# Optimization experiments

Measured on AMD Instinct MI355X. Metric: run time of the kernel, lower is better.

Reference implementation:

```python
import jax, jax.numpy as jnp
import numpy as np

# (top, left, bottom, right) box layout, per module constants
B, T, R, C = 32, 200, 4096, 81
REDUCTION = 16.0
IOU_THRESH = 0.7


def _make_boxes(key, b, n):
    k1, k2 = jax.random.split(key)
    cyx = jax.random.uniform(k1, (b, n, 2), minval=100.0, maxval=700.0)
    hw = jax.random.uniform(k2, (b, n, 2), minval=48.0, maxval=256.0)
    top = cyx[..., 0] - hw[..., 0] * 0.5
    left = cyx[..., 1] - hw[..., 1] * 0.5
    bottom = cyx[..., 0] + hw[..., 0] * 0.5
    right = cyx[..., 1] + hw[..., 1] * 0.5
    return jnp.stack([top, left, bottom, right], axis=-1)


def setup_inputs() -> dict:
    key = jax.random.key(0)
    ks = jax.random.split(key, 6)
    nms_reg = _make_boxes(ks[0], B, R)                              # [B,R,4] proposal boxes
    # ground-truth boxes: jittered copies of the first T proposals so many IoUs exceed 0.7
    bboxes = nms_reg[:, :T, :] + jax.random.normal(ks[1], (B, T, 4)) * 4.0
    classes = jax.random.randint(ks[2], (B, T), 0, C)               # [B,T] int labels
    rcnn_reg = jax.random.normal(ks[3], (B, R, 4)) * 0.1            # predicted box deltas
    rcnn_cls = jax.random.normal(ks[4], (B, R, C))                  # class logits
    nms_cls = jax.random.normal(ks[5], (B, R, 2))                   # unused by forward
    return {"nms_reg": nms_reg, "nms_cls": nms_cls, "rcnn_reg": rcnn_reg,
            "rcnn_cls": rcnn_cls, "bboxes": bboxes, "classes": classes}


def _iou(a, b):
    # a, b broadcastable [..., 4] in (top,left,bottom,right)
    t = jnp.maximum(a[..., 0], b[..., 0])
    l = jnp.maximum(a[..., 1], b[..., 1])
    bb = jnp.minimum(a[..., 2], b[..., 2])
    r = jnp.minimum(a[..., 3], b[..., 3])
    inter = jnp.clip(bb - t, 0.0) * jnp.clip(r - l, 0.0)
    area_a = (a[..., 2] - a[..., 0]) * (a[..., 3] - a[..., 1])
    area_b = (b[..., 2] - b[..., 0]) * (b[..., 3] - b[..., 1])
    return inter / (area_a + area_b - inter)


def reference(nms_reg, nms_cls, rcnn_reg, rcnn_cls, bboxes, classes):
    dt = rcnn_reg.dtype
    # pairwise IoU between proposals and GT boxes: [B, T, R]
    iou = _iou(nms_reg[:, None, :, :], bboxes[:, :, None, :])
    # torch sorts along T and takes the last slice == argmax over targets.
    # (gathers of rcnn_reg / rcnn_cls along T are identities since they are
    #  constant along T, so max_reg == rcnn_reg, max_rcnn_cls == rcnn_cls.)
    best = jnp.argmax(iou, axis=1)                                  # [B,R]
    max_iou = jnp.max(iou, axis=1)                                  # [B,R]
    max_bboxes = jnp.take_along_axis(bboxes, best[:, :, None], axis=1)   # [B,R,4]
    max_classes = jnp.take_along_axis(classes, best, axis=1)             # [B,R]

    mask = (max_iou > IOU_THRESH).astype(dt)                        # [B,R]
    npos = jnp.sum(mask)
    denom = jnp.maximum(npos, 1.0)

    # CrossEntropy over positives (mean reduction over masked elements)
    logp = jax.nn.log_softmax(rcnn_cls, axis=-1)
    ce = -jnp.take_along_axis(logp, max_classes[..., None], axis=-1)[..., 0]
    cls_loss = jnp.sum(ce * mask) / denom

    # categorical accuracy over positives
    acc = jnp.sum((jnp.argmax(rcnn_cls, axis=-1) == max_classes).astype(dt) * mask) / denom

    # normalized by rounded height/width
    rounded = jnp.round(max_bboxes / REDUCTION) * REDUCTION
    h = rounded[..., 2] - rounded[..., 0]
    w = rounded[..., 3] - rounded[..., 1]
    h = jnp.where(h == 0, 1.0, h)
    w = jnp.where(w == 0, 1.0, w)
    off = max_bboxes - rounded
    tgt = jnp.stack([off[..., 0] / h, off[..., 1] / w,
                     off[..., 2] / h, off[..., 3] / w], axis=-1)    # [B,R,4]

    d = jnp.abs(rcnn_reg - tgt)
    sl1 = jnp.where(d < 1.0, 0.5 * d * d, d - 0.5)
    # torch applies SmoothL1 (mean over positives) per coordinate, then sums
    reg_loss = jnp.sum(jnp.sum(sl1 * mask[..., None], axis=(0, 1)) / denom)

    has_pos = npos > 0
    z = jnp.zeros((), dt)
    return (jnp.where(has_pos, cls_loss, z),
            jnp.where(has_pos, reg_loss, z),
            jnp.where(has_pos, acc, z))
```

## Files before the change

### kernel.cpp

```cpp
#include <hip/hip_runtime.h>

#define BB 32
#define TT 200
#define RR 4096
#define CC 81
#define IOU_THRESH 0.7f
#define RED 16.0f

#define BLK 256
#define NBLOCKS (BB * (RR / BLK))

__global__ __launch_bounds__(BLK, 1) void rcnn_main_kernel(
    const float* __restrict__ nms_reg,
    const float* __restrict__ rcnn_reg,
    const float* __restrict__ rcnn_cls,
    const float* __restrict__ bboxes,
    const int*   __restrict__ classes,
    float* __restrict__ ws,
    float* __restrict__ out)
{
    __shared__ float4 s_box[TT];
    __shared__ float  s_area[TT];
    __shared__ int    s_cls[TT];
    __shared__ float  s_red[4][4];

    const int tid  = threadIdx.x;
    const int lane = tid & 63;
    const int blocks_per_b = RR / BLK;
    const int b = blockIdx.x / blocks_per_b;
    const int r = (blockIdx.x % blocks_per_b) * BLK + tid;
    const long gid = (long)b * RR + r;

    const float4* __restrict__ gbox = (const float4*)(bboxes + (long)b * TT * 4);
    for (int i = tid; i < TT; i += BLK) {
        const float4 g = gbox[i];
        s_box[i]  = g;
        s_area[i] = (g.z - g.x) * (g.w - g.y);
        s_cls[i]  = classes[b * TT + i];
    }
    __syncthreads();

    const float4 a = ((const float4*)nms_reg)[gid];
    const float area_a = (a.z - a.x) * (a.w - a.y);

    float bn = -1.0f, bd = 1.0f;
    int   bt = 0;
    #pragma unroll 8
    for (int t = 0; t < TT; ++t) {
        const float4 g = s_box[t];
        const float it = fmaxf(a.x, g.x);
        const float il = fmaxf(a.y, g.y);
        const float ib = fminf(a.z, g.z);
        const float ir = fminf(a.w, g.w);
        const float inter = fmaxf(ib - it, 0.0f) * fmaxf(ir - il, 0.0f);
        const float uni   = area_a + s_area[t] - inter;
        const bool better = inter * bd > bn * uni;
        bn = better ? inter : bn;
        bd = better ? uni   : bd;
        bt = better ? t     : bt;
    }

    const float pos = (bn > IOU_THRESH * bd) ? 1.0f : 0.0f;
    float ce = 0.0f, acc = 0.0f, reg = 0.0f;

    if (__ballot(pos > 0.5f) != 0ull) {
        const int cls = s_cls[bt];

        const float* __restrict__ row = rcnn_cls + gid * CC;
        float x[CC];
        #pragma unroll
        for (int c = 0; c < CC; ++c) x[c] = row[c];

        float m = x[0];
        int amax = 0;
        #pragma unroll
        for (int c = 1; c < CC; ++c) {
            if (x[c] > m) { m = x[c]; amax = c; }
        }
        float s = 0.0f;
        #pragma unroll
        for (int c = 0; c < CC; ++c) s += __expf(x[c] - m);
        const float xc = row[cls];
        ce  = (m + __logf(s) - xc) * pos;
        acc = (amax == cls) ? pos : 0.0f;

        const float4 g  = s_box[bt];
        const float4 pr = ((const float4*)rcnn_reg)[gid];
        const float rt = rintf(g.x / RED) * RED;
        const float rl = rintf(g.y / RED) * RED;
        const float rb = rintf(g.z / RED) * RED;
        const float rr = rintf(g.w / RED) * RED;
        float h = rb - rt; if (h == 0.0f) h = 1.0f;
        float w = rr - rl; if (w == 0.0f) w = 1.0f;
        const float d0 = fabsf(pr.x - (g.x - rt) / h);
        const float d1 = fabsf(pr.y - (g.y - rl) / w);
        const float d2 = fabsf(pr.z - (g.z - rb) / h);
        const float d3 = fabsf(pr.w - (g.w - rr) / w);
        float sl  = (d0 < 1.0f) ? 0.5f * d0 * d0 : d0 - 0.5f;
        sl += (d1 < 1.0f) ? 0.5f * d1 * d1 : d1 - 0.5f;
        sl += (d2 < 1.0f) ? 0.5f * d2 * d2 : d2 - 0.5f;
        sl += (d3 < 1.0f) ? 0.5f * d3 * d3 : d3 - 0.5f;
        reg = sl * pos;
    }

    float p4 = pos, e4 = ce, a4 = acc, g4 = reg;
    #pragma unroll
    for (int off = 32; off > 0; off >>= 1) {
        p4 += __shfl_down(p4, off);
        e4 += __shfl_down(e4, off);
        a4 += __shfl_down(a4, off);
        g4 += __shfl_down(g4, off);
    }
    const int wave = tid >> 6;
    if (lane == 0) {
        s_red[wave][0] = p4;
        s_red[wave][1] = e4;
        s_red[wave][2] = a4;
        s_red[wave][3] = g4;
    }
    __syncthreads();
    if (tid == 0) {
        float P = 0.0f, E = 0.0f, A = 0.0f, G = 0.0f;
        #pragma unroll
        for (int v = 0; v < 4; ++v) {
            P += s_red[v][0];
            E += s_red[v][1];
            A += s_red[v][2];
            G += s_red[v][3];
        }
        atomicAdd(&ws[0], P);
        atomicAdd(&ws[1], E);
        atomicAdd(&ws[2], A);
        atomicAdd(&ws[3], G);
        __threadfence();
        unsigned int* cnt = (unsigned int*)&ws[4];
        const unsigned int old = atomicAdd(cnt, 1u);
        if (old == (unsigned int)(gridDim.x - 1)) {
            const float npos = atomicAdd(&ws[0], 0.0f);
            const float sce  = atomicAdd(&ws[1], 0.0f);
            const float sac  = atomicAdd(&ws[2], 0.0f);
            const float srg  = atomicAdd(&ws[3], 0.0f);
            const float denom = fmaxf(npos, 1.0f);
            const bool  hp = npos > 0.0f;
            out[0] = hp ? sce / denom : 0.0f;
            out[1] = hp ? srg / denom : 0.0f;
            out[2] = hp ? sac / denom : 0.0f;
        }
    }
}

extern "C" void kernel_launch(void* const* d_in, const int* in_sizes, int n_in,
                              void* d_out, int out_size, void* d_ws, size_t ws_size,
                              hipStream_t stream) {
    const float* nms_reg  = (const float*)d_in[0];
    const float* rcnn_reg = (const float*)d_in[2];
    const float* rcnn_cls = (const float*)d_in[3];
    const float* bboxes   = (const float*)d_in[4];
    const int*   classes  = (const int*)d_in[5];
    float* ws  = (float*)d_ws;
    float* out = (float*)d_out;

    hipMemsetAsync(ws, 0, 8 * sizeof(float), stream);
    rcnn_main_kernel<<<NBLOCKS, BLK, 0, stream>>>(
        nms_reg, rcnn_reg, rcnn_cls, bboxes, classes, ws, out);
}
```

Before: 134.6 us.

## Split IoU matching and softmax cross-entropy into two kernels via per-proposal flags

Splits the fused kernel into two. The first computes IoU matching, regression loss and per-block partial sums, and writes a byte flag per proposal holding the matched target index. The second reads the flags and computes cross-entropy and accuracy only for positive proposals. Each kernel reduces into the workspace, and the last block of the second kernel combines everything. This removes the memset, cuts register pressure in the IoU loop by moving the 81-float logits array into its own kernel, and lets only lanes with positives load logits, at the cost of an extra launch and a flag array round trip through memory.

After: 132.7 us. Within noise of the previous version (-1.4%).

```diff
diff --git a/kernel.cpp b/kernel.cpp
--- a/kernel.cpp
+++ b/kernel.cpp
@@ -8,21 +8,19 @@
 #define RED 16.0f
 
 #define BLK 256
-#define NBLOCKS (BB * (RR / BLK))
-
-__global__ __launch_bounds__(BLK, 1) void rcnn_main_kernel(
+#define NB (BB * (RR / BLK))
+
+#define WS_PART_OFF 16
+#define WS_FLAG_OFF 8192
+
+__global__ __launch_bounds__(BLK) void rcnn_k1(
     const float* __restrict__ nms_reg,
     const float* __restrict__ rcnn_reg,
-    const float* __restrict__ rcnn_cls,
     const float* __restrict__ bboxes,
-    const int*   __restrict__ classes,
-    float* __restrict__ ws,
-    float* __restrict__ out)
+    unsigned char* __restrict__ ws)
 {
     __shared__ float4 s_box[TT];
-    __shared__ float  s_area[TT];
-    __shared__ int    s_cls[TT];
-    __shared__ float  s_red[4][4];
+    __shared__ float  s_red[4][2];
 
     const int tid  = threadIdx.x;
     const int lane = tid & 63;
@@ -32,12 +30,7 @@
     const long gid = (long)b * RR + r;
 
     const float4* __restrict__ gbox = (const float4*)(bboxes + (long)b * TT * 4);
-    for (int i = tid; i < TT; i += BLK) {
-        const float4 g = gbox[i];
-        s_box[i]  = g;
-        s_area[i] = (g.z - g.x) * (g.w - g.y);
-        s_cls[i]  = classes[b * TT + i];
-    }
+    for (int i = tid; i < TT; i += BLK) s_box[i] = gbox[i];
     __syncthreads();
 
     const float4 a = ((const float4*)nms_reg)[gid];
@@ -53,36 +46,19 @@
         const float ib = fminf(a.z, g.z);
         const float ir = fminf(a.w, g.w);
         const float inter = fmaxf(ib - it, 0.0f) * fmaxf(ir - il, 0.0f);
-        const float uni   = area_a + s_area[t] - inter;
+        const float uni   = area_a + (g.z - g.x) * (g.w - g.y) - inter;
         const bool better = inter * bd > bn * uni;
         bn = better ? inter : bn;
         bd = better ? uni   : bd;
         bt = better ? t     : bt;
     }
 
-    const float pos = (bn > IOU_THRESH * bd) ? 1.0f : 0.0f;
-    float ce = 0.0f, acc = 0.0f, reg = 0.0f;
-
-    if (__ballot(pos > 0.5f) != 0ull) {
-        const int cls = s_cls[bt];
-
-        const float* __restrict__ row = rcnn_cls + gid * CC;
-        float x[CC];
-        #pragma unroll
-        for (int c = 0; c < CC; ++c) x[c] = row[c];
-
-        float m = x[0];
-        int amax = 0;
-        #pragma unroll
-        for (int c = 1; c < CC; ++c) {
-            if (x[c] > m) { m = x[c]; amax = c; }
-        }
-        float s = 0.0f;
-        #pragma unroll
-        for (int c = 0; c < CC; ++c) s += __expf(x[c] - m);
-        const float xc = row[cls];
-        ce  = (m + __logf(s) - xc) * pos;
-        acc = (amax == cls) ? pos : 0.0f;
+    const bool ispos = (bn > IOU_THRESH * bd);
+    float pos = 0.0f, reg = 0.0f;
+    unsigned char flag = 0;
+    if (ispos) {
+        pos  = 1.0f;
+        flag = (unsigned char)(bt + 1);
 
         const float4 g  = s_box[bt];
         const float4 pr = ((const float4*)rcnn_reg)[gid];
@@ -96,54 +72,123 @@
         const float d1 = fabsf(pr.y - (g.y - rl) / w);
         const float d2 = fabsf(pr.z - (g.z - rb) / h);
         const float d3 = fabsf(pr.w - (g.w - rr) / w);
-        float sl  = (d0 < 1.0f) ? 0.5f * d0 * d0 : d0 - 0.5f;
-        sl += (d1 < 1.0f) ? 0.5f * d1 * d1 : d1 - 0.5f;
-        sl += (d2 < 1.0f) ? 0.5f * d2 * d2 : d2 - 0.5f;
-        sl += (d3 < 1.0f) ? 0.5f * d3 * d3 : d3 - 0.5f;
-        reg = sl * pos;
-    }
-
-    float p4 = pos, e4 = ce, a4 = acc, g4 = reg;
+        reg  = (d0 < 1.0f) ? 0.5f * d0 * d0 : d0 - 0.5f;
+        reg += (d1 < 1.0f) ? 0.5f * d1 * d1 : d1 - 0.5f;
+        reg += (d2 < 1.0f) ? 0.5f * d2 * d2 : d2 - 0.5f;
+        reg += (d3 < 1.0f) ? 0.5f * d3 * d3 : d3 - 0.5f;
+    }
+    (ws + WS_FLAG_OFF)[gid] = flag;
+
     #pragma unroll
     for (int off = 32; off > 0; off >>= 1) {
-        p4 += __shfl_down(p4, off);
-        e4 += __shfl_down(e4, off);
-        a4 += __shfl_down(a4, off);
-        g4 += __shfl_down(g4, off);
+        pos += __shfl_down(pos, off);
+        reg += __shfl_down(reg, off);
     }
     const int wave = tid >> 6;
-    if (lane == 0) {
-        s_red[wave][0] = p4;
-        s_red[wave][1] = e4;
-        s_red[wave][2] = a4;
-        s_red[wave][3] = g4;
-    }
+    if (lane == 0) { s_red[wave][0] = pos; s_red[wave][1] = reg; }
     __syncthreads();
     if (tid == 0) {
-        float P = 0.0f, E = 0.0f, A = 0.0f, G = 0.0f;
-        #pragma unroll
-        for (int v = 0; v < 4; ++v) {
-            P += s_red[v][0];
-            E += s_red[v][1];
-            A += s_red[v][2];
-            G += s_red[v][3];
-        }
-        atomicAdd(&ws[0], P);
-        atomicAdd(&ws[1], E);
-        atomicAdd(&ws[2], A);
-        atomicAdd(&ws[3], G);
+        float P = 0.0f, G = 0.0f;
+        #pragma unroll
+        for (int v = 0; v < 4; ++v) { P += s_red[v][0]; G += s_red[v][1]; }
+        float2* part = (float2*)(ws + WS_PART_OFF);
+        part[blockIdx.x] = make_float2(P, G);
+        if (blockIdx.x == 0) {
+            *(unsigned int*)ws = 0u;
+            *(float*)(ws + 4) = 0.0f;
+            *(float*)(ws + 8) = 0.0f;
+        }
+    }
+}
+
+__global__ __launch_bounds__(BLK) void rcnn_k2(
+    const float* __restrict__ rcnn_cls,
+    const int*   __restrict__ classes,
+    unsigned char* __restrict__ ws,
+    float* __restrict__ out)
+{
+    __shared__ float s_red[4][2];
+    __shared__ int   s_last;
+
+    const int tid  = threadIdx.x;
+    const int lane = tid & 63;
+    const int blocks_per_b = RR / BLK;
+    const int b = blockIdx.x / blocks_per_b;
+    const int r = (blockIdx.x % blocks_per_b) * BLK + tid;
+    const long gid = (long)b * RR + r;
+
+    const int f = (ws + WS_FLAG_OFF)[gid];
+    float ce = 0.0f, acc = 0.0f;
+    if (f != 0) {
+        const int bt  = f - 1;
+        const int cls = classes[b * TT + bt];
+        const float* __restrict__ row = rcnn_cls + gid * CC;
+
+        float x[CC];
+        #pragma unroll
+        for (int c = 0; c < CC; ++c) x[c] = row[c];
+
+        float m = x[0];
+        int amax = 0;
+        #pragma unroll
+        for (int c = 1; c < CC; ++c) {
+            if (x[c] > m) { m = x[c]; amax = c; }
+        }
+        float s = 0.0f;
+        #pragma unroll
+        for (int c = 0; c < CC; ++c) s += __expf(x[c] - m);
+        const float xc = row[cls];
+        ce  = m + __logf(s) - xc;
+        acc = (amax == cls) ? 1.0f : 0.0f;
+    }
+
+    #pragma unroll
+    for (int off = 32; off > 0; off >>= 1) {
+        ce  += __shfl_down(ce,  off);
+        acc += __shfl_down(acc, off);
+    }
+    const int wave = tid >> 6;
+    if (lane == 0) { s_red[wave][0] = ce; s_red[wave][1] = acc; }
+    __syncthreads();
+
+    float* ws_ce  = (float*)(ws + 4);
+    float* ws_acc = (float*)(ws + 8);
+    if (tid == 0) {
+        float E = 0.0f, A = 0.0f;
+        #pragma unroll
+        for (int v = 0; v < 4; ++v) { E += s_red[v][0]; A += s_red[v][1]; }
+        atomicAdd(ws_ce,  E);
+        atomicAdd(ws_acc, A);
         __threadfence();
-        unsigned int* cnt = (unsigned int*)&ws[4];
-        const unsigned int old = atomicAdd(cnt, 1u);
-        if (old == (unsigned int)(gridDim.x - 1)) {
-            const float npos = atomicAdd(&ws[0], 0.0f);
-            const float sce  = atomicAdd(&ws[1], 0.0f);
-            const float sac  = atomicAdd(&ws[2], 0.0f);
-            const float srg  = atomicAdd(&ws[3], 0.0f);
-            const float denom = fmaxf(npos, 1.0f);
-            const bool  hp = npos > 0.0f;
+        const unsigned int old = atomicAdd((unsigned int*)ws, 1u);
+        s_last = (old == (unsigned int)(gridDim.x - 1)) ? 1 : 0;
+    }
+    __syncthreads();
+
+    if (s_last) {
+        const float2* part = (const float2*)(ws + WS_PART_OFF);
+        float np = 0.0f, rg = 0.0f;
+        for (int i = tid; i < NB; i += BLK) {
+            const float2 p = part[i];
+            np += p.x; rg += p.y;
+        }
+        #pragma unroll
+        for (int off = 32; off > 0; off >>= 1) {
+            np += __shfl_down(np, off);
+            rg += __shfl_down(rg, off);
+        }
+        if (lane == 0) { s_red[wave][0] = np; s_red[wave][1] = rg; }
+        __syncthreads();
+        if (tid == 0) {
+            float P = 0.0f, G = 0.0f;
+            #pragma unroll
+            for (int v = 0; v < 4; ++v) { P += s_red[v][0]; G += s_red[v][1]; }
+            const float sce = atomicAdd(ws_ce,  0.0f);
+            const float sac = atomicAdd(ws_acc, 0.0f);
+            const float denom = fmaxf(P, 1.0f);
+            const bool  hp = P > 0.0f;
             out[0] = hp ? sce / denom : 0.0f;
-            out[1] = hp ? srg / denom : 0.0f;
+            out[1] = hp ? G   / denom : 0.0f;
             out[2] = hp ? sac / denom : 0.0f;
         }
     }
@@ -157,10 +202,9 @@
     const float* rcnn_cls = (const float*)d_in[3];
     const float* bboxes   = (const float*)d_in[4];
     const int*   classes  = (const int*)d_in[5];
-    float* ws  = (float*)d_ws;
+    unsigned char* ws = (unsigned char*)d_ws;
     float* out = (float*)d_out;
 
-    hipMemsetAsync(ws, 0, 8 * sizeof(float), stream);
-    rcnn_main_kernel<<<NBLOCKS, BLK, 0, stream>>>(
-        nms_reg, rcnn_reg, rcnn_cls, bboxes, classes, ws, out);
+    rcnn_k1<<<NB, BLK, 0, stream>>>(nms_reg, rcnn_reg, bboxes, ws);
+    rcnn_k2<<<NB, BLK, 0, stream>>>(rcnn_cls, classes, ws, out);
 }
```
